# Kernel tuning notes

Measured on AMD Instinct MI355X. Metric: run time of the kernel, lower is better.

## Reference

```python
import jax, jax.numpy as jnp
import numpy as np

B, S, D, EXP = 2, 2048, 128, 16
N = D * EXP  # state_dim = 2048


def setup_inputs() -> dict:
    key = jax.random.key(0)
    ks = jax.random.split(key, 11)
    s_in = 1.0 / np.sqrt(D)   # torch Linear default init bound for dim->N layers
    s_out = 1.0 / np.sqrt(N)  # for out_proj (N->dim)
    x = jax.random.normal(ks[0], (B, S, D), dtype=jnp.float32)
    W_B = jax.random.uniform(ks[1], (N, D), jnp.float32, -s_in, s_in)
    b_B = jax.random.uniform(ks[2], (N,), jnp.float32, -s_in, s_in)
    W_C = jax.random.uniform(ks[3], (N, D), jnp.float32, -s_in, s_in)
    b_C = jax.random.uniform(ks[4], (N,), jnp.float32, -s_in, s_in)
    W_dt = jax.random.uniform(ks[5], (N, D), jnp.float32, -s_in, s_in)
    b_dt = jax.random.uniform(ks[6], (N,), jnp.float32, -s_in, s_in)
    A_log = jnp.log(jax.random.uniform(ks[7], (N,), jnp.float32) * 0.5 + 0.5)
    W_out = jax.random.uniform(ks[8], (D, N), jnp.float32, -s_out, s_out)
    b_out = jax.random.uniform(ks[9], (D,), jnp.float32, -s_out, s_out)
    return {"x": x, "W_B": W_B, "b_B": b_B, "W_C": W_C, "b_C": b_C,
            "W_dt": W_dt, "b_dt": b_dt, "A_log": A_log,
            "W_out": W_out, "b_out": b_out}


def reference(x, W_B, b_B, W_C, b_C, W_dt, b_dt, A_log, W_out, b_out):
    # Featurizer projections: [B,S,D] -> [B,S,N]
    B_feat = jnp.einsum('bsd,nd->bsn', x, W_B) + b_B
    C_feat = jnp.einsum('bsd,nd->bsn', x, W_C) + b_C
    dt = jax.nn.softplus(jnp.einsum('bsd,nd->bsn', x, W_dt) + b_dt)
    A = -jnp.exp(A_log)                # [N]
    A_bar = jnp.exp(dt * A)            # [B,S,N]
    B_bar = dt * B_feat                # [B,S,N]

    # Sequential diagonal scan: h_t = A_t * h_{t-1} + B_t ; y_t = C_t * h_t
    def step(h, abc):
        a_t, b_t, c_t = abc            # each [B,N]
        h = a_t * h + b_t
        return h, c_t * h

    h0 = jnp.zeros((x.shape[0], N), dtype=x.dtype)
    xs = (jnp.swapaxes(A_bar, 0, 1),   # [S,B,N]
          jnp.swapaxes(B_bar, 0, 1),
          jnp.swapaxes(C_feat, 0, 1))
    _, ys = jax.lax.scan(step, h0, xs)  # ys: [S,B,N]
    y = jnp.swapaxes(ys, 0, 1)          # [B,S,N]
    return jnp.einsum('bsn,dn->bsd', y, W_out) + b_out
```

## Files before the change

### kernel.cpp

```cpp
#include <hip/hip_runtime.h>


#define BB 2
#define SS 2048
#define DDIM 128
#define NDIM 2048
#define TT (BB*SS)
#define NTILE (TT/16)

typedef short short8 __attribute__((ext_vector_type(8)));
typedef float floatx4 __attribute__((ext_vector_type(4)));

__device__ __forceinline__ unsigned short f2b(float f){
  unsigned u = __float_as_uint(f);
  u += 0x7FFFu + ((u >> 16) & 1u);
  return (unsigned short)(u >> 16);
}
__device__ __forceinline__ unsigned cvt_pk_bf16(float lo, float hi){
  unsigned r;
  asm("v_cvt_pk_bf16_f32 %0, %1, %2" : "=v"(r) : "v"(lo), "v"(hi));
  return r;
}
__device__ __forceinline__ float softplus_f(float v){
  return v > 15.f ? v : __logf(1.f + __expf(v));
}
__device__ __forceinline__ void pack8(const float* __restrict__ s,
                                      unsigned short* __restrict__ d){
  floatx4 v0 = *(const floatx4*)s;
  floatx4 v1 = *(const floatx4*)(s + 4);
  short8 r;
  r[0]=(short)f2b(v0[0]); r[1]=(short)f2b(v0[1]); r[2]=(short)f2b(v0[2]); r[3]=(short)f2b(v0[3]);
  r[4]=(short)f2b(v1[0]); r[5]=(short)f2b(v1[1]); r[6]=(short)f2b(v1[2]); r[7]=(short)f2b(v1[3]);
  *(short8*)d = r;
}

__global__ void prep_kernel(const float* __restrict__ x,
                            const float* __restrict__ W_B,
                            const float* __restrict__ W_C,
                            const float* __restrict__ W_dt,
                            const float* __restrict__ A_log,
                            const float* __restrict__ W_out,
                            unsigned short* __restrict__ xp,
                            unsigned short* __restrict__ Wp3,
                            unsigned short* __restrict__ Wop,
                            float* __restrict__ Aval,
                            unsigned long long* __restrict__ Sbuf){
  const int gid = blockIdx.x * blockDim.x + threadIdx.x;
  if (gid < 32768) Sbuf[gid] = 0ull;
  if (gid < 2048) Aval[gid] = -__expf(A_log[gid]);
  if (gid < 65536){
    int g = gid, tile = g >> 8, kk = (g >> 6) & 3, lane = g & 63;
    int q = lane >> 4, m = lane & 15;
    pack8(x + (size_t)(tile*16 + m)*DDIM + kk*32 + q*8, xp + (size_t)g*8);
  }
  if (gid < 98304){
    int mat = gid >> 15, g = gid & 32767;
    const float* W = (mat == 0) ? W_B : (mat == 1 ? W_dt : W_C);
    int tile = g >> 8, kk = (g >> 6) & 3, lane = g & 63;
    int q = lane >> 4, m = lane & 15;
    pack8(W + (size_t)(tile*16 + m)*DDIM + kk*32 + q*8,
          Wp3 + (size_t)mat*262144 + (size_t)g*8);
  }
  if (gid < 32768){
    int g = gid, tile = g >> 12, kk = (g >> 6) & 63, lane = g & 63;
    int q = lane >> 4, m = lane & 15;
    pack8(W_out + (size_t)(tile*16 + m)*NDIM + kk*32 + q*8, Wop + (size_t)g*8);
  }
}

__global__ __launch_bounds__(256, 2) void projscan_kernel(
    const unsigned short* __restrict__ xp,
    const unsigned short* __restrict__ Wp3,
    const float* __restrict__ b_B,
    const float* __restrict__ b_dt,
    const float* __restrict__ b_C,
    const float* __restrict__ Aval,
    unsigned long long* __restrict__ Sbuf,
    unsigned short* __restrict__ ybp){
  __shared__ unsigned short sW[3*4096];
  __shared__ unsigned short sYT[4][640];
  __shared__ float sPw[4][32], sHw[4][32];
  __shared__ float sIw[4][32];
  const int tid  = threadIdx.x;
  const int lane = tid & 63;
  const int wv   = tid >> 6;
  const int m    = lane & 15;
  const int q    = lane >> 4;
  const int p    = blockIdx.y * 16 + blockIdx.x;
  const int xcd  = p & 7;
  const int slot = p >> 3;
  const int rr   = slot & 15;
  const int j    = slot >> 4;
  const int row  = xcd*16 + rr;
  const int by   = row >> 1;
  const int bx   = (row & 1)*8 + j;
  const int n0   = by*32;

  for (int i = tid; i < 1536; i += 256){
    int mat = i >> 9, rem = i & 511;
    *(short8*)(sW + mat*4096 + rem*8) =
        *(const short8*)(Wp3 + (size_t)mat*262144 + (size_t)by*4096 + rem*8);
  }
  __syncthreads();

  float bBv[2], bDv[2], bCv[2], Avv[2];
#pragma unroll
  for (int nt = 0; nt < 2; ++nt){
    const int n = n0 + nt*16 + m;
    bBv[nt] = b_B[n]; bDv[nt] = b_dt[n]; bCv[nt] = b_C[n]; Avv[nt] = Aval[n];
  }

  float pa_run[2] = {1.f, 1.f}, ha_run[2] = {0.f, 0.f};
#pragma unroll
  for (int i = 0; i < 4; ++i){
    const int tile = bx*16 + wv*4 + i;
    short8 xf[4];
#pragma unroll
    for (int kk = 0; kk < 4; ++kk)
      xf[kk] = *(const short8*)(xp + (size_t)tile*2048 + kk*512 + lane*8);

    floatx4 aB[2], aD[2];
#pragma unroll
    for (int nt = 0; nt < 2; ++nt){
      aB[nt] = (floatx4){0.f,0.f,0.f,0.f};
      aD[nt] = (floatx4){0.f,0.f,0.f,0.f};
    }
#pragma unroll
    for (int nt = 0; nt < 2; ++nt)
#pragma unroll
      for (int kk = 0; kk < 4; ++kk){
        short8 wB = *(const short8*)(sW +         nt*2048 + kk*512 + lane*8);
        short8 wD = *(const short8*)(sW + 4096 +  nt*2048 + kk*512 + lane*8);
        aB[nt] = __builtin_amdgcn_mfma_f32_16x16x32_bf16(xf[kk], wB, aB[nt], 0, 0, 0);
        aD[nt] = __builtin_amdgcn_mfma_f32_16x16x32_bf16(xf[kk], wD, aD[nt], 0, 0, 0);
      }

#pragma unroll
    for (int nt = 0; nt < 2; ++nt){
      float P, H;
      {
        float Ar[4], Br[4];
#pragma unroll
        for (int r = 0; r < 4; ++r){
          float dtv = softplus_f(aD[nt][r] + bDv[nt]);
          Ar[r] = __expf(dtv * Avv[nt]);
          Br[r] = dtv * (aB[nt][r] + bBv[nt]);
        }
        P = Ar[0]; H = Br[0];
#pragma unroll
        for (int r = 1; r < 4; ++r){ H = Ar[r]*H + Br[r]; P *= Ar[r]; }
      }
      float pp = __shfl(P, (lane - 16) & 63, 64);
      float hh = __shfl(H, (lane - 16) & 63, 64);
      if (q >= 1){ H = P*hh + H; P *= pp; }
      pp = __shfl(P, (lane - 32) & 63, 64);
      hh = __shfl(H, (lane - 32) & 63, 64);
      if (q >= 2){ H = P*hh + H; P *= pp; }
      float pb = __shfl(P, m + 48, 64);
      float hb = __shfl(H, m + 48, 64);
      ha_run[nt] = pb*ha_run[nt] + hb;
      pa_run[nt] *= pb;
    }
  }
  if (q == 0){
#pragma unroll
    for (int nt = 0; nt < 2; ++nt){
      sPw[wv][nt*16 + m] = pa_run[nt];
      sHw[wv][nt*16 + m] = ha_run[nt];
    }
  }
  __syncthreads();

  if (tid < 32){
    float Pw[4], Hw[4];
#pragma unroll
    for (int w2 = 0; w2 < 4; ++w2){ Pw[w2] = sPw[w2][tid]; Hw[w2] = sHw[w2][tid]; }
    float pb = 1.f, hb = 0.f;
#pragma unroll
    for (int w2 = 0; w2 < 4; ++w2){ hb = Pw[w2]*hb + Hw[w2]; pb *= Pw[w2]; }
    float pbc = fmaxf(pb, 1e-30f);
    __hip_atomic_store(Sbuf + (size_t)(by*16 + bx)*32 + tid,
        ((unsigned long long)__float_as_uint(pbc) << 32) |
         (unsigned long long)__float_as_uint(hb),
        __ATOMIC_RELAXED, __HIP_MEMORY_SCOPE_AGENT);
    float S = 0.f;
    const int cnt = bx & 7;
    if (cnt){
      const int j0 = bx & ~7;
      unsigned long long v0=0,v1=0,v2=0,v3=0,v4=0,v5=0,v6=0;
      unsigned got = 0;
      int spin = 0;
      const unsigned all = (1u << cnt) - 1u;
      const unsigned long long* base = Sbuf + (size_t)(by*16 + j0)*32 + tid;
      for (;;){
#define LOOKBACK(J, V)                                                          \
        if (J < cnt && !(got & (1u << J))){                                     \
          unsigned long long a = __hip_atomic_load(base + (size_t)J*32,         \
              __ATOMIC_RELAXED, __HIP_MEMORY_SCOPE_AGENT);                      \
          if ((unsigned)(a >> 32) != 0u){ V = a; got |= 1u << J; }              \
        }
        LOOKBACK(0, v0) LOOKBACK(1, v1) LOOKBACK(2, v2) LOOKBACK(3, v3)
        LOOKBACK(4, v4) LOOKBACK(5, v5) LOOKBACK(6, v6)
#undef LOOKBACK
        if (got == all) break;
        if (spin < 4) __builtin_amdgcn_s_sleep(2);
        else          __builtin_amdgcn_s_sleep(8);
        ++spin;
      }
#define COMPOSE(J, V)                                                           \
      if (J < cnt) S = __uint_as_float((unsigned)(V >> 32))*S +                 \
                       __uint_as_float((unsigned)V);
      COMPOSE(0, v0) COMPOSE(1, v1) COMPOSE(2, v2) COMPOSE(3, v3)
      COMPOSE(4, v4) COMPOSE(5, v5) COMPOSE(6, v6)
#undef COMPOSE
    }
    float s = S;
#pragma unroll
    for (int w2 = 0; w2 < 4; ++w2){
      sIw[w2][tid] = s;
      s = Pw[w2]*s + Hw[w2];
    }
  }
  __syncthreads();

  float it_run[2];
#pragma unroll
  for (int nt = 0; nt < 2; ++nt) it_run[nt] = sIw[wv][nt*16 + m];

#pragma unroll
  for (int i = 0; i < 4; ++i){
    const int tile = bx*16 + wv*4 + i;
    short8 xf[4];
#pragma unroll
    for (int kk = 0; kk < 4; ++kk)
      xf[kk] = *(const short8*)(xp + (size_t)tile*2048 + kk*512 + lane*8);

    floatx4 acc[3][2];
#pragma unroll
    for (int mat = 0; mat < 3; ++mat)
#pragma unroll
      for (int nt = 0; nt < 2; ++nt)
        acc[mat][nt] = (floatx4){0.f,0.f,0.f,0.f};
#pragma unroll
    for (int nt = 0; nt < 2; ++nt)
#pragma unroll
      for (int kk = 0; kk < 4; ++kk){
        short8 wB = *(const short8*)(sW +         nt*2048 + kk*512 + lane*8);
        short8 wD = *(const short8*)(sW + 4096 +  nt*2048 + kk*512 + lane*8);
        short8 wC = *(const short8*)(sW + 8192 +  nt*2048 + kk*512 + lane*8);
        acc[0][nt] = __builtin_amdgcn_mfma_f32_16x16x32_bf16(xf[kk], wB, acc[0][nt], 0, 0, 0);
        acc[1][nt] = __builtin_amdgcn_mfma_f32_16x16x32_bf16(xf[kk], wD, acc[1][nt], 0, 0, 0);
        acc[2][nt] = __builtin_amdgcn_mfma_f32_16x16x32_bf16(xf[kk], wC, acc[2][nt], 0, 0, 0);
      }

#pragma unroll
    for (int nt = 0; nt < 2; ++nt){
      float Ar[4], Br[4], Cc[4];
#pragma unroll
      for (int r = 0; r < 4; ++r){
        float dtv = softplus_f(acc[1][nt][r] + bDv[nt]);
        Ar[r] = __expf(dtv * Avv[nt]);
        Br[r] = dtv * (acc[0][nt][r] + bBv[nt]);
        Cc[r] = acc[2][nt][r] + bCv[nt];
      }
      float P = Ar[0], H = Br[0];
#pragma unroll
      for (int r = 1; r < 4; ++r){ H = Ar[r]*H + Br[r]; P *= Ar[r]; }
      float pp = __shfl(P, (lane - 16) & 63, 64);
      float hh = __shfl(H, (lane - 16) & 63, 64);
      if (q >= 1){ H = P*hh + H; P *= pp; }
      pp = __shfl(P, (lane - 32) & 63, 64);
      hh = __shfl(H, (lane - 32) & 63, 64);
      if (q >= 2){ H = P*hh + H; P *= pp; }
      float pe = __shfl(P, (lane - 16) & 63, 64);
      float he = __shfl(H, (lane - 16) & 63, 64);
      if (q == 0){ pe = 1.f; he = 0.f; }
      float pb = __shfl(P, m + 48, 64);
      float hb = __shfl(H, m + 48, 64);

      float h = pe*it_run[nt] + he;
      float ys[4];
#pragma unroll
      for (int r = 0; r < 4; ++r){
        h = Ar[r]*h + Br[r];
        ys[r] = Cc[r]*h;
      }
      unsigned y01 = cvt_pk_bf16(ys[0], ys[1]);
      unsigned y23 = cvt_pk_bf16(ys[2], ys[3]);
      sYT[wv][(q*4 + 0)*40 + nt*16 + m] = (unsigned short)(y01);
      sYT[wv][(q*4 + 1)*40 + nt*16 + m] = (unsigned short)(y01 >> 16);
      sYT[wv][(q*4 + 2)*40 + nt*16 + m] = (unsigned short)(y23);
      sYT[wv][(q*4 + 3)*40 + nt*16 + m] = (unsigned short)(y23 >> 16);

      it_run[nt] = pb*it_run[nt] + hb;
    }
    short8 yv = *(const short8*)&sYT[wv][m*40 + q*8];
    *(short8*)(ybp + (size_t)tile*32768 + (size_t)by*512 + (size_t)lane*8) = yv;
  }
}

__global__ __launch_bounds__(512, 1) void outproj_kernel(
    const unsigned short* __restrict__ ybp,
    const unsigned short* __restrict__ Wop,
    const float* __restrict__ b_out,
    float* __restrict__ out){
  __shared__ float red[8*2048];
  const int tid  = threadIdx.x;
  const int lane = tid & 63;
  const int wv   = tid >> 6;
  const int m    = lane & 15;
  const int q    = lane >> 4;
  const int tile = blockIdx.x;

  floatx4 acc[8];
#pragma unroll
  for (int dt = 0; dt < 8; ++dt) acc[dt] = (floatx4){0.f,0.f,0.f,0.f};

  const unsigned short* aP = ybp + (size_t)tile*32768 + lane*8;
  const unsigned short* bP = Wop + (size_t)lane*8;
#pragma unroll
  for (int kk = wv*8; kk < wv*8 + 8; ++kk){
    short8 af = *(const short8*)(aP + (size_t)kk*512);
#pragma unroll
    for (int dt = 0; dt < 8; ++dt){
      short8 bf = *(const short8*)(bP + (size_t)dt*32768 + (size_t)kk*512);
      acc[dt] = __builtin_amdgcn_mfma_f32_16x16x32_bf16(af, bf, acc[dt], 0, 0, 0);
    }
  }
#pragma unroll
  for (int dt = 0; dt < 8; ++dt)
#pragma unroll
    for (int r = 0; r < 4; ++r)
      red[wv*2048 + (q*4 + r)*128 + dt*16 + m] = acc[dt][r];
  __syncthreads();
#pragma unroll
  for (int i = 0; i < 4; ++i){
    int idx = i*512 + tid;
    float s = red[idx]          + red[2048 + idx] + red[4096 + idx] + red[6144 + idx]
            + red[8192 + idx]   + red[10240 + idx] + red[12288 + idx] + red[14336 + idx];
    int tl = idx >> 7, d = idx & 127;
    out[(size_t)(tile*16 + tl)*DDIM + d] = s + b_out[d];
  }
}

extern "C" void kernel_launch(void* const* d_in, const int* in_sizes, int n_in,
                              void* d_out, int out_size, void* d_ws, size_t ws_size,
                              hipStream_t stream) {
  const float* x     = (const float*)d_in[0];
  const float* W_B   = (const float*)d_in[1];
  const float* b_B   = (const float*)d_in[2];
  const float* W_C   = (const float*)d_in[3];
  const float* b_C   = (const float*)d_in[4];
  const float* W_dt  = (const float*)d_in[5];
  const float* b_dt  = (const float*)d_in[6];
  const float* A_log = (const float*)d_in[7];
  const float* W_out = (const float*)d_in[8];
  const float* b_out = (const float*)d_in[9];
  float* out = (float*)d_out;

  char* w = (char*)d_ws;
  unsigned short* xp    = (unsigned short*)(w + 0x0000000);
  unsigned short* Wp3   = (unsigned short*)(w + 0x0100000);
  unsigned short* Wop   = (unsigned short*)(w + 0x0280000);
  float*          Aval  = (float*)         (w + 0x0300000);
  unsigned short* ybp   = (unsigned short*)(w + 0x0310000);
  unsigned long long* Sbuf = (unsigned long long*)(w + 0x1310000);

  prep_kernel<<<384, 256, 0, stream>>>(
      x, W_B, W_C, W_dt, A_log, W_out, xp, Wp3, Wop, Aval, Sbuf);

  projscan_kernel<<<dim3(16, 64), 256, 0, stream>>>(
      xp, Wp3, b_B, b_dt, b_C, Aval, Sbuf, ybp);

  outproj_kernel<<<NTILE, 512, 0, stream>>>(ybp, Wop, b_out, out);
}
```

Baseline: 118.3 us.

## Replace decoupled lookback with three-pass chunked scan and shrink outproj blocks

Splits the fused projection+scan kernel into three kernels. The first computes per-wave chunk aggregates. A small kernel sequentially scans those aggregates into carry-in values, and the second recomputes the B/dt projections plus C to apply the carries. This removes the spin-wait lookback on atomics and the XCD-aware block remapping, at the cost of recomputing the B/dt projections and two extra launches. The out-projection kernel also drops to 256 threads with 16 k-steps per wave.

```diff
diff --git a/kernel.cpp b/kernel.cpp
--- a/kernel.cpp
+++ b/kernel.cpp
@@ -43,10 +43,8 @@
                             unsigned short* __restrict__ xp,
                             unsigned short* __restrict__ Wp3,
                             unsigned short* __restrict__ Wop,
-                            float* __restrict__ Aval,
-                            unsigned long long* __restrict__ Sbuf){
+                            float* __restrict__ Aval){
   const int gid = blockIdx.x * blockDim.x + threadIdx.x;
-  if (gid < 32768) Sbuf[gid] = 0ull;
   if (gid < 2048) Aval[gid] = -__expf(A_log[gid]);
   if (gid < 65536){
     int g = gid, tile = g >> 8, kk = (g >> 6) & 3, lane = g & 63;
@@ -68,46 +66,35 @@
   }
 }
 
-__global__ __launch_bounds__(256, 2) void projscan_kernel(
+__global__ __launch_bounds__(256, 2) void pass1_kernel(
     const unsigned short* __restrict__ xp,
     const unsigned short* __restrict__ Wp3,
     const float* __restrict__ b_B,
     const float* __restrict__ b_dt,
-    const float* __restrict__ b_C,
     const float* __restrict__ Aval,
-    unsigned long long* __restrict__ Sbuf,
-    unsigned short* __restrict__ ybp){
-  __shared__ unsigned short sW[3*4096];
-  __shared__ unsigned short sYT[4][640];
-  __shared__ float sPw[4][32], sHw[4][32];
-  __shared__ float sIw[4][32];
+    float2* __restrict__ Wagg){
+  __shared__ unsigned short sW[2*4096];
   const int tid  = threadIdx.x;
   const int lane = tid & 63;
   const int wv   = tid >> 6;
   const int m    = lane & 15;
   const int q    = lane >> 4;
-  const int p    = blockIdx.y * 16 + blockIdx.x;
-  const int xcd  = p & 7;
-  const int slot = p >> 3;
-  const int rr   = slot & 15;
-  const int j    = slot >> 4;
-  const int row  = xcd*16 + rr;
-  const int by   = row >> 1;
-  const int bx   = (row & 1)*8 + j;
+  const int bx   = blockIdx.x;
+  const int by   = blockIdx.y;
   const int n0   = by*32;
 
-  for (int i = tid; i < 1536; i += 256){
+  for (int i = tid; i < 1024; i += 256){
     int mat = i >> 9, rem = i & 511;
     *(short8*)(sW + mat*4096 + rem*8) =
         *(const short8*)(Wp3 + (size_t)mat*262144 + (size_t)by*4096 + rem*8);
   }
   __syncthreads();
 
-  float bBv[2], bDv[2], bCv[2], Avv[2];
+  float bBv[2], bDv[2], Avv[2];
 #pragma unroll
   for (int nt = 0; nt < 2; ++nt){
     const int n = n0 + nt*16 + m;
-    bBv[nt] = b_B[n]; bDv[nt] = b_dt[n]; bCv[nt] = b_C[n]; Avv[nt] = Aval[n];
+    bBv[nt] = b_B[n]; bDv[nt] = b_dt[n]; Avv[nt] = Aval[n];
   }
 
   float pa_run[2] = {1.f, 1.f}, ha_run[2] = {0.f, 0.f};
@@ -129,27 +116,24 @@
     for (int nt = 0; nt < 2; ++nt)
 #pragma unroll
       for (int kk = 0; kk < 4; ++kk){
-        short8 wB = *(const short8*)(sW +         nt*2048 + kk*512 + lane*8);
-        short8 wD = *(const short8*)(sW + 4096 +  nt*2048 + kk*512 + lane*8);
+        short8 wB = *(const short8*)(sW +        nt*2048 + kk*512 + lane*8);
+        short8 wD = *(const short8*)(sW + 4096 + nt*2048 + kk*512 + lane*8);
         aB[nt] = __builtin_amdgcn_mfma_f32_16x16x32_bf16(xf[kk], wB, aB[nt], 0, 0, 0);
         aD[nt] = __builtin_amdgcn_mfma_f32_16x16x32_bf16(xf[kk], wD, aD[nt], 0, 0, 0);
       }
 
 #pragma unroll
     for (int nt = 0; nt < 2; ++nt){
-      float P, H;
-      {
-        float Ar[4], Br[4];
-#pragma unroll
-        for (int r = 0; r < 4; ++r){
-          float dtv = softplus_f(aD[nt][r] + bDv[nt]);
-          Ar[r] = __expf(dtv * Avv[nt]);
-          Br[r] = dtv * (aB[nt][r] + bBv[nt]);
-        }
-        P = Ar[0]; H = Br[0];
-#pragma unroll
-        for (int r = 1; r < 4; ++r){ H = Ar[r]*H + Br[r]; P *= Ar[r]; }
-      }
+      float Ar[4], Br[4];
+#pragma unroll
+      for (int r = 0; r < 4; ++r){
+        float dtv = softplus_f(aD[nt][r] + bDv[nt]);
+        Ar[r] = __expf(dtv * Avv[nt]);
+        Br[r] = dtv * (aB[nt][r] + bBv[nt]);
+      }
+      float P = Ar[0], H = Br[0];
+#pragma unroll
+      for (int r = 1; r < 4; ++r){ H = Ar[r]*H + Br[r]; P *= Ar[r]; }
       float pp = __shfl(P, (lane - 16) & 63, 64);
       float hh = __shfl(H, (lane - 16) & 63, 64);
       if (q >= 1){ H = P*hh + H; P *= pp; }
@@ -164,68 +148,65 @@
   }
   if (q == 0){
 #pragma unroll
-    for (int nt = 0; nt < 2; ++nt){
-      sPw[wv][nt*16 + m] = pa_run[nt];
-      sHw[wv][nt*16 + m] = ha_run[nt];
-    }
+    for (int nt = 0; nt < 2; ++nt)
+      Wagg[(size_t)((by*16 + bx)*4 + wv)*32 + nt*16 + m] =
+          make_float2(pa_run[nt], ha_run[nt]);
+  }
+}
+
+__global__ void scan_kernel(const float2* __restrict__ Wagg,
+                            float* __restrict__ Ibuf){
+  const int c  = blockIdx.x * 256 + threadIdx.x;
+  const int n  = c & 31;
+  const int ch = c >> 5;
+  const int by = ch >> 1;
+  const int b  = ch & 1;
+  const size_t base = (size_t)((by*16 + b*8)*4)*32 + n;
+  float2 v[32];
+#pragma unroll
+  for (int k = 0; k < 32; ++k) v[k] = Wagg[base + (size_t)k*32];
+  float S = 0.f;
+#pragma unroll
+  for (int k = 0; k < 32; ++k){
+    Ibuf[base + (size_t)k*32] = S;
+    S = v[k].x*S + v[k].y;
+  }
+}
+
+__global__ __launch_bounds__(256, 2) void pass2_kernel(
+    const unsigned short* __restrict__ xp,
+    const unsigned short* __restrict__ Wp3,
+    const float* __restrict__ b_B,
+    const float* __restrict__ b_dt,
+    const float* __restrict__ b_C,
+    const float* __restrict__ Aval,
+    const float* __restrict__ Ibuf,
+    unsigned short* __restrict__ ybp){
+  __shared__ unsigned short sW[3*4096];
+  __shared__ unsigned short sYT[4][640];
+  const int tid  = threadIdx.x;
+  const int lane = tid & 63;
+  const int wv   = tid >> 6;
+  const int m    = lane & 15;
+  const int q    = lane >> 4;
+  const int bx   = blockIdx.x;
+  const int by   = blockIdx.y;
+  const int n0   = by*32;
+
+  for (int i = tid; i < 1536; i += 256){
+    int mat = i >> 9, rem = i & 511;
+    *(short8*)(sW + mat*4096 + rem*8) =
+        *(const short8*)(Wp3 + (size_t)mat*262144 + (size_t)by*4096 + rem*8);
   }
   __syncthreads();
 
-  if (tid < 32){
-    float Pw[4], Hw[4];
-#pragma unroll
-    for (int w2 = 0; w2 < 4; ++w2){ Pw[w2] = sPw[w2][tid]; Hw[w2] = sHw[w2][tid]; }
-    float pb = 1.f, hb = 0.f;
-#pragma unroll
-    for (int w2 = 0; w2 < 4; ++w2){ hb = Pw[w2]*hb + Hw[w2]; pb *= Pw[w2]; }
-    float pbc = fmaxf(pb, 1e-30f);
-    __hip_atomic_store(Sbuf + (size_t)(by*16 + bx)*32 + tid,
-        ((unsigned long long)__float_as_uint(pbc) << 32) |
-         (unsigned long long)__float_as_uint(hb),
-        __ATOMIC_RELAXED, __HIP_MEMORY_SCOPE_AGENT);
-    float S = 0.f;
-    const int cnt = bx & 7;
-    if (cnt){
-      const int j0 = bx & ~7;
-      unsigned long long v0=0,v1=0,v2=0,v3=0,v4=0,v5=0,v6=0;
-      unsigned got = 0;
-      int spin = 0;
-      const unsigned all = (1u << cnt) - 1u;
-      const unsigned long long* base = Sbuf + (size_t)(by*16 + j0)*32 + tid;
-      for (;;){
-#define LOOKBACK(J, V)                                                          \
-        if (J < cnt && !(got & (1u << J))){                                     \
-          unsigned long long a = __hip_atomic_load(base + (size_t)J*32,         \
-              __ATOMIC_RELAXED, __HIP_MEMORY_SCOPE_AGENT);                      \
-          if ((unsigned)(a >> 32) != 0u){ V = a; got |= 1u << J; }              \
-        }
-        LOOKBACK(0, v0) LOOKBACK(1, v1) LOOKBACK(2, v2) LOOKBACK(3, v3)
-        LOOKBACK(4, v4) LOOKBACK(5, v5) LOOKBACK(6, v6)
-#undef LOOKBACK
-        if (got == all) break;
-        if (spin < 4) __builtin_amdgcn_s_sleep(2);
-        else          __builtin_amdgcn_s_sleep(8);
-        ++spin;
-      }
-#define COMPOSE(J, V)                                                           \
-      if (J < cnt) S = __uint_as_float((unsigned)(V >> 32))*S +                 \
-                       __uint_as_float((unsigned)V);
-      COMPOSE(0, v0) COMPOSE(1, v1) COMPOSE(2, v2) COMPOSE(3, v3)
-      COMPOSE(4, v4) COMPOSE(5, v5) COMPOSE(6, v6)
-#undef COMPOSE
-    }
-    float s = S;
-#pragma unroll
-    for (int w2 = 0; w2 < 4; ++w2){
-      sIw[w2][tid] = s;
-      s = Pw[w2]*s + Hw[w2];
-    }
-  }
-  __syncthreads();
-
-  float it_run[2];
-#pragma unroll
-  for (int nt = 0; nt < 2; ++nt) it_run[nt] = sIw[wv][nt*16 + m];
+  float bBv[2], bDv[2], bCv[2], Avv[2], it_run[2];
+#pragma unroll
+  for (int nt = 0; nt < 2; ++nt){
+    const int n = n0 + nt*16 + m;
+    bBv[nt] = b_B[n]; bDv[nt] = b_dt[n]; bCv[nt] = b_C[n]; Avv[nt] = Aval[n];
+    it_run[nt] = Ibuf[(size_t)((by*16 + bx)*4 + wv)*32 + nt*16 + m];
+  }
 
 #pragma unroll
   for (int i = 0; i < 4; ++i){
@@ -299,12 +280,11 @@
   }
 }
 
-__global__ __launch_bounds__(512, 1) void outproj_kernel(
-    const unsigned short* __restrict__ ybp,
-    const unsigned short* __restrict__ Wop,
-    const float* __restrict__ b_out,
-    float* __restrict__ out){
-  __shared__ float red[8*2048];
+__global__ void outproj_kernel(const unsigned short* __restrict__ ybp,
+                               const unsigned short* __restrict__ Wop,
+                               const float* __restrict__ b_out,
+                               float* __restrict__ out){
+  __shared__ float red[4*2048];
   const int tid  = threadIdx.x;
   const int lane = tid & 63;
   const int wv   = tid >> 6;
@@ -318,8 +298,8 @@
 
   const unsigned short* aP = ybp + (size_t)tile*32768 + lane*8;
   const unsigned short* bP = Wop + (size_t)lane*8;
-#pragma unroll
-  for (int kk = wv*8; kk < wv*8 + 8; ++kk){
+#pragma unroll 4
+  for (int kk = wv*16; kk < wv*16 + 16; ++kk){
     short8 af = *(const short8*)(aP + (size_t)kk*512);
 #pragma unroll
     for (int dt = 0; dt < 8; ++dt){
@@ -334,10 +314,9 @@
       red[wv*2048 + (q*4 + r)*128 + dt*16 + m] = acc[dt][r];
   __syncthreads();
 #pragma unroll
-  for (int i = 0; i < 4; ++i){
-    int idx = i*512 + tid;
-    float s = red[idx]          + red[2048 + idx] + red[4096 + idx] + red[6144 + idx]
-            + red[8192 + idx]   + red[10240 + idx] + red[12288 + idx] + red[14336 + idx];
+  for (int i = 0; i < 8; ++i){
+    int idx = i*256 + tid;
+    float s = red[idx] + red[2048 + idx] + red[4096 + idx] + red[6144 + idx];
     int tl = idx >> 7, d = idx & 127;
     out[(size_t)(tile*16 + tl)*DDIM + d] = s + b_out[d];
   }
@@ -364,13 +343,19 @@
   unsigned short* Wop   = (unsigned short*)(w + 0x0280000);
   float*          Aval  = (float*)         (w + 0x0300000);
   unsigned short* ybp   = (unsigned short*)(w + 0x0310000);
-  unsigned long long* Sbuf = (unsigned long long*)(w + 0x1310000);
+  float2*         Wagg  = (float2*)        (w + 0x1310000);
+  float*          Ibuf  = (float*)         (w + 0x1410000);
 
   prep_kernel<<<384, 256, 0, stream>>>(
-      x, W_B, W_C, W_dt, A_log, W_out, xp, Wp3, Wop, Aval, Sbuf);
-
-  projscan_kernel<<<dim3(16, 64), 256, 0, stream>>>(
-      xp, Wp3, b_B, b_dt, b_C, Aval, Sbuf, ybp);
-
-  outproj_kernel<<<NTILE, 512, 0, stream>>>(ybp, Wop, b_out, out);
-}
+      x, W_B, W_C, W_dt, A_log, W_out, xp, Wp3, Wop, Aval);
+
+  pass1_kernel<<<dim3(16, 64), 256, 0, stream>>>(
+      xp, Wp3, b_B, b_dt, Aval, Wagg);
+
+  scan_kernel<<<16, 256, 0, stream>>>(Wagg, Ibuf);
+
+  pass2_kernel<<<dim3(16, 64), 256, 0, stream>>>(
+      xp, Wp3, b_B, b_dt, b_C, Aval, Ibuf, ybp);
+
+  outproj_kernel<<<NTILE, 256, 0, stream>>>(ybp, Wop, b_out, out);
+}
```

New measurement: 124.6 us. 1.05x slower.
